# Kernel tuning notes

Measured on AMD Instinct MI355X. Metric: run time of the kernel, lower is better.

Reference implementation:

```python
import jax, jax.numpy as jnp
import numpy as np

SEQ_LEN = 8192
HEAD_DIM = 128


def setup_inputs() -> dict:
    key = jax.random.key(0)
    kq, kk, kv = jax.random.split(key, 3)
    q = jax.random.normal(kq, (SEQ_LEN, HEAD_DIM), dtype=jnp.float32)
    k = jax.random.normal(kk, (SEQ_LEN, HEAD_DIM), dtype=jnp.float32)
    v = jax.random.normal(kv, (SEQ_LEN, HEAD_DIM), dtype=jnp.float32)
    return {"q": q, "k": k, "v": v}


def reference(q, k, v):
    # FlashAttention computes exact softmax attention; the blocked loops with
    # online max/sum rescaling in the source are an exact reformulation of:
    #   O = softmax(Q K^T) V
    # NOTE: the original module applies no 1/sqrt(d) scaling, so neither do we.
    s = jnp.einsum('nd,md->nm', q, k)          # [N, N] scores
    p = jax.nn.softmax(s, axis=-1)             # stable softmax (online in src)
    return jnp.einsum('nm,md->nd', p, v)       # [N, d]
```

## Files before the change

kernel.cpp:

```cpp
#include <hip/hip_runtime.h>

#define N_SEQ 8192
#define HDIM  128

typedef _Float16 half8v  __attribute__((ext_vector_type(8)));
typedef float    floatx16 __attribute__((ext_vector_type(16)));
typedef unsigned int uint32;

__global__ void prep_kv(const float* __restrict__ K, const float* __restrict__ V,
                        _Float16* __restrict__ K16s, _Float16* __restrict__ Vs) {
    __shared__ float Kl[32 * 132];
    __shared__ float Vl[32 * 132];
    const int t  = threadIdx.x;
    const int nt = blockIdx.x;
    const int n0 = nt * 32;
    #pragma unroll
    for (int kk = 0; kk < 4; kk++) {
        int idx = t + 256 * kk;
        int nl = idx >> 5, c4 = idx & 31;
        float4 f = *(((const float4*)(K + (size_t)(n0 + nl) * HDIM)) + c4);
        float* dk = &Kl[nl * 132 + c4 * 4];
        dk[0] = f.x; dk[1] = f.y; dk[2] = f.z; dk[3] = f.w;
        float4 g = *(((const float4*)(V + (size_t)(n0 + nl) * HDIM)) + c4);
        float* dv = &Vl[nl * 132 + c4 * 4];
        dv[0] = g.x; dv[1] = g.y; dv[2] = g.z; dv[3] = g.w;
    }
    __syncthreads();
    #pragma unroll
    for (int rep = 0; rep < 2; rep++) {
        int ch = t + rep * 256;
        int kc = ch >> 6, lane = ch & 63, l31 = lane & 31, q5 = (lane >> 5) & 1;
        half8v h;
        #pragma unroll
        for (int j = 0; j < 8; j++) h[j] = (_Float16)Kl[l31 * 132 + kc * 16 + q5 * 8 + j];
        *(half8v*)(K16s + (((size_t)nt * 8 + kc) * 64 + lane) * 8) = h;
    }
    #pragma unroll
    for (int rep = 0; rep < 2; rep++) {
        int ch = t + rep * 256;
        int dt = ch >> 7, kc2 = (ch >> 6) & 1, lane = ch & 63, l31 = lane & 31, q5 = (lane >> 5) & 1;
        half8v h;
        #pragma unroll
        for (int j = 0; j < 8; j++) h[j] = (_Float16)Vl[(kc2 * 16 + q5 * 8 + j) * 132 + dt * 32 + l31];
        *(half8v*)(Vs + ((((size_t)nt * 4 + dt) * 2 + kc2) * 64 + lane) * 8) = h;
    }
}

static __device__ __forceinline__ void stage_tile(
        const _Float16* __restrict__ K16s, const _Float16* __restrict__ Vs,
        _Float16* lds, size_t nt, int wv, int lane) {
    #pragma unroll
    for (int i = 0; i < 4; i++) {
        const int c = wv * 4 + i;
        const _Float16* base = (c < 8) ? (K16s + (nt * 8 + c) * 512)
                                       : (Vs + (nt * 8 + (size_t)(c - 8)) * 512);
        __builtin_amdgcn_global_load_lds(
            (const __attribute__((address_space(1))) void*)(base + lane * 8),
            (__attribute__((address_space(3))) void*)(lds + c * 512),
            16, 0, 0);
    }
}

static __device__ __forceinline__ void do_pv(const half8v (&vsrc)[8], const uint32 (&hpk)[8],
                                             floatx16 (&oacc)[4], int q5) {
    #pragma unroll
    for (int kc2 = 0; kc2 < 2; kc2++) {
        uint32 pass0 = q5 ? hpk[4 * kc2 + 0] : hpk[4 * kc2 + 2];
        uint32 pass1 = q5 ? hpk[4 * kc2 + 1] : hpk[4 * kc2 + 3];
        uint32 r0 = (uint32)__shfl_xor((int)pass0, 32, 64);
        uint32 r1 = (uint32)__shfl_xor((int)pass1, 32, 64);
        uint32 b0 = q5 ? r0 : hpk[4 * kc2 + 0];
        uint32 b1 = q5 ? r1 : hpk[4 * kc2 + 1];
        uint32 b2 = q5 ? hpk[4 * kc2 + 2] : r0;
        uint32 b3 = q5 ? hpk[4 * kc2 + 3] : r1;
        uint4 bu = make_uint4(b0, b1, b2, b3);
        half8v bfrag = __builtin_bit_cast(half8v, bu);
        #pragma unroll
        for (int dt = 0; dt < 4; dt++)
            oacc[dt] = __builtin_amdgcn_mfma_f32_32x32x16_f16(vsrc[dt * 2 + kc2], bfrag, oacc[dt], 0, 0, 0);
    }
}

template <bool DO_PV>
static __device__ __forceinline__ void pipe_step(
        const half8v (&qf)[8], half8v (&vin)[8], const half8v (&vprev)[8],
        floatx16 (&oacc)[4], uint32 (&hpk)[8],
        float& runm, float& lsum, float& palpha, bool& pflag,
        const _Float16* lds, int lane, int q5) {
    half8v kf[8];
    #pragma unroll
    for (int kc = 0; kc < 8; kc++)
        kf[kc] = *(const half8v*)(lds + kc * 512 + lane * 8);
    #pragma unroll
    for (int j = 0; j < 8; j++)
        vin[j] = *(const half8v*)(lds + (8 + j) * 512 + lane * 8);
    if (pflag) {
        #pragma unroll
        for (int dt = 0; dt < 4; dt++)
            #pragma unroll
            for (int r = 0; r < 16; r++) oacc[dt][r] *= palpha;
        pflag = false;
    }
    if (DO_PV) do_pv(vprev, hpk, oacc, q5);
    floatx16 s0, s1;
    #pragma unroll
    for (int r = 0; r < 16; r++) { s0[r] = 0.0f; s1[r] = 0.0f; }
    #pragma unroll
    for (int kc = 0; kc < 4; kc++)
        s0 = __builtin_amdgcn_mfma_f32_32x32x16_f16(kf[kc], qf[kc], s0, 0, 0, 0);
    #pragma unroll
    for (int kc = 4; kc < 8; kc++)
        s1 = __builtin_amdgcn_mfma_f32_32x32x16_f16(kf[kc], qf[kc], s1, 0, 0, 0);
    float sc[16];
    #pragma unroll
    for (int r = 0; r < 16; r++) sc[r] = s0[r] + s1[r];
    float tm[8];
    #pragma unroll
    for (int r = 0; r < 8; r++) tm[r] = fmaxf(sc[r], sc[r + 8]);
    #pragma unroll
    for (int w = 4; w; w >>= 1)
        #pragma unroll
        for (int r = 0; r < w; r++) tm[r] = fmaxf(tm[r], tm[r + w]);
    float cmax = fmaxf(tm[0], __shfl_xor(tm[0], 32, 64));
    if (__any(cmax > runm + 12.0f)) {
        const float mnew = fmaxf(runm, cmax);
        palpha = __builtin_amdgcn_exp2f(runm - mnew);
        runm = mnew;
        lsum *= palpha;
        pflag = true;
    }
    float p[16];
    #pragma unroll
    for (int r = 0; r < 16; r++) p[r] = __builtin_amdgcn_exp2f(sc[r] - runm);
    float ts[8];
    #pragma unroll
    for (int r = 0; r < 8; r++) ts[r] = p[r] + p[r + 8];
    #pragma unroll
    for (int w = 4; w; w >>= 1)
        #pragma unroll
        for (int r = 0; r < w; r++) ts[r] += ts[r + w];
    lsum += ts[0];
    #pragma unroll
    for (int t2 = 0; t2 < 8; t2++) {
        auto pk = __builtin_amdgcn_cvt_pkrtz(p[2 * t2], p[2 * t2 + 1]);
        hpk[t2] = __builtin_bit_cast(uint32, pk);
    }
}

__launch_bounds__(256, 2)
__global__ void fa_main(const float* __restrict__ Qp, const _Float16* __restrict__ K16s,
                        const _Float16* __restrict__ Vs, float* __restrict__ Opart,
                        float* __restrict__ lpart, float* __restrict__ mpart, int tiles) {
    __shared__ _Float16 ldsbuf[2][8192];
    const int tid  = threadIdx.x;
    const int lane = tid & 63;
    const int wv   = tid >> 6;
    const int l31  = lane & 31;
    const int q5   = lane >> 5;
    const int sp   = blockIdx.x;
    const int m0   = blockIdx.y * 128 + wv * 32;
    const float LOG2E = 1.44269504088896f;

    half8v qf[8];
    {
        const float* qrow = Qp + (size_t)(m0 + l31) * HDIM;
        #pragma unroll
        for (int kc = 0; kc < 8; kc++) {
            const float4 a = *(const float4*)(qrow + kc * 16 + q5 * 8);
            const float4 b = *(const float4*)(qrow + kc * 16 + q5 * 8 + 4);
            half8v h;
            h[0] = (_Float16)(a.x * LOG2E); h[1] = (_Float16)(a.y * LOG2E);
            h[2] = (_Float16)(a.z * LOG2E); h[3] = (_Float16)(a.w * LOG2E);
            h[4] = (_Float16)(b.x * LOG2E); h[5] = (_Float16)(b.y * LOG2E);
            h[6] = (_Float16)(b.z * LOG2E); h[7] = (_Float16)(b.w * LOG2E);
            qf[kc] = h;
        }
    }

    floatx16 oacc[4];
    #pragma unroll
    for (int dt = 0; dt < 4; dt++)
        #pragma unroll
        for (int r = 0; r < 16; r++) oacc[dt][r] = 0.0f;

    float runm = -3.0e38f;
    float lsum = 0.0f;
    float palpha = 0.0f;
    bool  pflag = false;
    uint32 hpk[8];
    half8v va[8], vb[8];

    const size_t nt0 = (size_t)sp * tiles;

    stage_tile(K16s, Vs, ldsbuf[0], nt0, wv, lane);
    __syncthreads();
    stage_tile(K16s, Vs, ldsbuf[1], nt0 + 1, wv, lane);
    pipe_step<false>(qf, va, va, oacc, hpk, runm, lsum, palpha, pflag, ldsbuf[0], lane, q5);
    __syncthreads();
    for (int p = 0; p < (tiles - 2) / 2; p++) {
        stage_tile(K16s, Vs, ldsbuf[0], nt0 + 2 + 2 * p, wv, lane);
        pipe_step<true>(qf, vb, va, oacc, hpk, runm, lsum, palpha, pflag, ldsbuf[1], lane, q5);
        __syncthreads();
        stage_tile(K16s, Vs, ldsbuf[1], nt0 + 3 + 2 * p, wv, lane);
        pipe_step<true>(qf, va, vb, oacc, hpk, runm, lsum, palpha, pflag, ldsbuf[0], lane, q5);
        __syncthreads();
    }
    pipe_step<true>(qf, vb, va, oacc, hpk, runm, lsum, palpha, pflag, ldsbuf[1], lane, q5);
    if (pflag) {
        #pragma unroll
        for (int dt = 0; dt < 4; dt++)
            #pragma unroll
            for (int r = 0; r < 16; r++) oacc[dt][r] *= palpha;
    }
    do_pv(vb, hpk, oacc, q5);

    float ltot = lsum + __shfl_xor(lsum, 32, 64);
    if (lane < 32) {
        lpart[(size_t)sp * N_SEQ + m0 + l31] = ltot;
        mpart[(size_t)sp * N_SEQ + m0 + l31] = runm;
    }

    float* ldsf = (float*)ldsbuf;
    const size_t obase = ((size_t)sp * N_SEQ + blockIdx.y * 128) * HDIM;
    #pragma unroll
    for (int qtr = 0; qtr < 4; qtr++) {
        __syncthreads();
        if (wv == qtr) {
            #pragma unroll
            for (int dt = 0; dt < 4; dt++)
                #pragma unroll
                for (int g = 0; g < 4; g++) {
                    float4 v = make_float4(oacc[dt][4 * g + 0], oacc[dt][4 * g + 1],
                                           oacc[dt][4 * g + 2], oacc[dt][4 * g + 3]);
                    *(float4*)&ldsf[l31 * 132 + dt * 32 + g * 8 + q5 * 4] = v;
                }
        }
        __syncthreads();
        const int lrow = wv * 8 + (lane >> 3);
        const int c    = lane & 7;
        #pragma unroll
        for (int j = 0; j < 4; j++) {
            float4 v = *(const float4*)&ldsf[lrow * 132 + (j * 8 + c) * 4];
            *(float4*)&Opart[obase + (size_t)(qtr * 32 + lrow) * HDIM + (j * 8 + c) * 4] = v;
        }
    }
}

template <int S>
__global__ __launch_bounds__(256) void fa_merge(const float* __restrict__ Opart,
                                                const float* __restrict__ lpart,
                                                const float* __restrict__ mpart,
                                                float* __restrict__ Out) {
    const int t = threadIdx.x;
    const int m = blockIdx.x * 32 + (t >> 3);
    const int c = t & 7;

    float mv[S], lv[S];
    #pragma unroll
    for (int s = 0; s < S; s++) {
        mv[s] = mpart[(size_t)s * N_SEQ + m];
        lv[s] = lpart[(size_t)s * N_SEQ + m];
    }
    float M = -3.0e38f;
    #pragma unroll
    for (int s = 0; s < S; s++) M = fmaxf(M, mv[s]);
    float wsc[S];
    float L = 0.0f;
    #pragma unroll
    for (int s = 0; s < S; s++) {
        wsc[s] = __builtin_amdgcn_exp2f(mv[s] - M);
        L += lv[s] * wsc[s];
    }
    const float inv = 1.0f / L;

    float4 acc[4];
    #pragma unroll
    for (int j = 0; j < 4; j++) acc[j] = make_float4(0.f, 0.f, 0.f, 0.f);
    #pragma unroll
    for (int s = 0; s < S; s++) {
        const float ww = wsc[s] * inv;
        const float* src = Opart + ((size_t)s * N_SEQ + m) * HDIM;
        #pragma unroll
        for (int j = 0; j < 4; j++) {
            float4 v = *(const float4*)&src[(j * 8 + c) * 4];
            acc[j].x += v.x * ww; acc[j].y += v.y * ww;
            acc[j].z += v.z * ww; acc[j].w += v.w * ww;
        }
    }
    float* dst = Out + (size_t)m * HDIM;
    #pragma unroll
    for (int j = 0; j < 4; j++)
        *(float4*)&dst[(j * 8 + c) * 4] = acc[j];
}

__global__ void fa_naive(const float* __restrict__ Q, const float* __restrict__ K,
                         const float* __restrict__ V, float* __restrict__ O) {
    const int m = blockIdx.x;
    const int t = threadIdx.x;
    __shared__ float qs[HDIM];
    __shared__ float ps[256];
    __shared__ float red[256];
    if (t < HDIM) qs[t] = Q[(size_t)m * HDIM + t] * 1.44269504f;
    __syncthreads();
    float om = -3.0e38f, ls = 0.0f, oa = 0.0f;
    for (int nb = 0; nb < N_SEQ; nb += 256) {
        const float* kr = K + (size_t)(nb + t) * HDIM;
        float s = 0.0f;
        #pragma unroll 8
        for (int d = 0; d < HDIM; d++) s += qs[d] * kr[d];
        red[t] = s; __syncthreads();
        for (int st = 128; st > 0; st >>= 1) { if (t < st) red[t] = fmaxf(red[t], red[t + st]); __syncthreads(); }
        float cm = red[0];
        __syncthreads();
        float mn = fmaxf(om, cm);
        float al = __builtin_amdgcn_exp2f(om - mn);
        om = mn;
        float pp = __builtin_amdgcn_exp2f(s - mn);
        ps[t] = pp; red[t] = pp; __syncthreads();
        for (int st = 128; st > 0; st >>= 1) { if (t < st) red[t] += red[t + st]; __syncthreads(); }
        float csum = red[0];
        ls = ls * al + csum;
        if (t < HDIM) {
            float acc = 0.0f;
            for (int j = 0; j < 256; j++) acc += ps[j] * V[(size_t)(nb + j) * HDIM + t];
            oa = oa * al + acc;
        }
        __syncthreads();
    }
    if (t < HDIM) O[(size_t)m * HDIM + t] = oa / ls;
}

extern "C" void kernel_launch(void* const* d_in, const int* in_sizes, int n_in,
                              void* d_out, int out_size, void* d_ws, size_t ws_size,
                              hipStream_t stream) {
    const float* q = (const float*)d_in[0];
    const float* k = (const float*)d_in[1];
    const float* v = (const float*)d_in[2];
    float* out = (float*)d_out;

    const size_t MB = 1024ull * 1024ull;
    int S = 0;
    for (int s = 8; s >= 1; s >>= 1) {
        size_t need = 4 * MB + (size_t)s * (4 * MB + 64 * 1024);
        if (ws_size >= need) { S = s; break; }
    }
    if (S == 0) {
        fa_naive<<<N_SEQ, 256, 0, stream>>>(q, k, v, out);
        return;
    }
    char* ws = (char*)d_ws;
    _Float16* K16s = (_Float16*)ws;
    _Float16* Vs   = (_Float16*)(ws + 2 * MB);
    float* Opart   = (float*)(ws + 4 * MB);
    float* lpart   = (float*)(ws + 4 * MB + (size_t)S * 4 * MB);
    float* mpart   = lpart + (size_t)S * N_SEQ;

    prep_kv<<<dim3(N_SEQ / 32), dim3(256), 0, stream>>>(k, v, K16s, Vs);
    fa_main<<<dim3(S, N_SEQ / 128), dim3(256), 0, stream>>>(q, K16s, Vs, Opart, lpart, mpart, (N_SEQ / 32) / S);
    dim3 mg(N_SEQ / 32);
    switch (S) {
        case 8:  fa_merge<8> <<<mg, dim3(256), 0, stream>>>(Opart, lpart, mpart, out); break;
        case 4:  fa_merge<4> <<<mg, dim3(256), 0, stream>>>(Opart, lpart, mpart, out); break;
        case 2:  fa_merge<2> <<<mg, dim3(256), 0, stream>>>(Opart, lpart, mpart, out); break;
        default: fa_merge<1> <<<mg, dim3(256), 0, stream>>>(Opart, lpart, mpart, out); break;
    }
}
```

Baseline: 120.8 us.

## Triple-buffer K/V LDS staging with partial waitcnt barriers and widen merge grid

```diff
diff --git a/kernel.cpp b/kernel.cpp
--- a/kernel.cpp
+++ b/kernel.cpp
@@ -147,11 +147,16 @@
     }
 }
 
+static __device__ __forceinline__ void phase_sync() {
+    asm volatile("s_waitcnt vmcnt(4) lgkmcnt(0)" ::: "memory");
+    __builtin_amdgcn_s_barrier();
+}
+
 __launch_bounds__(256, 2)
 __global__ void fa_main(const float* __restrict__ Qp, const _Float16* __restrict__ K16s,
                         const _Float16* __restrict__ Vs, float* __restrict__ Opart,
                         float* __restrict__ lpart, float* __restrict__ mpart, int tiles) {
-    __shared__ _Float16 ldsbuf[2][8192];
+    __shared__ _Float16 ldsbuf[3][8192];
     const int tid  = threadIdx.x;
     const int lane = tid & 63;
     const int wv   = tid >> 6;
@@ -191,21 +196,37 @@
     half8v va[8], vb[8];
 
     const size_t nt0 = (size_t)sp * tiles;
-
-    stage_tile(K16s, Vs, ldsbuf[0], nt0, wv, lane);
-    __syncthreads();
-    stage_tile(K16s, Vs, ldsbuf[1], nt0 + 1, wv, lane);
-    pipe_step<false>(qf, va, va, oacc, hpk, runm, lsum, palpha, pflag, ldsbuf[0], lane, q5);
-    __syncthreads();
+    _Float16* lb = &ldsbuf[0][0];
+    const int last = tiles - 1;
+
+    stage_tile(K16s, Vs, lb + 0 * 8192, nt0 + 0, wv, lane);
+    stage_tile(K16s, Vs, lb + 1 * 8192, nt0 + 1, wv, lane);
+
+    phase_sync();
+    stage_tile(K16s, Vs, lb + 2 * 8192, nt0 + 2, wv, lane);
+    pipe_step<false>(qf, va, va, oacc, hpk, runm, lsum, palpha, pflag, lb, lane, q5);
+
+    int cs = 1;
+    int ps = 0;
     for (int p = 0; p < (tiles - 2) / 2; p++) {
-        stage_tile(K16s, Vs, ldsbuf[0], nt0 + 2 + 2 * p, wv, lane);
-        pipe_step<true>(qf, vb, va, oacc, hpk, runm, lsum, palpha, pflag, ldsbuf[1], lane, q5);
-        __syncthreads();
-        stage_tile(K16s, Vs, ldsbuf[1], nt0 + 3 + 2 * p, wv, lane);
-        pipe_step<true>(qf, va, vb, oacc, hpk, runm, lsum, palpha, pflag, ldsbuf[0], lane, q5);
-        __syncthreads();
-    }
-    pipe_step<true>(qf, vb, va, oacc, hpk, runm, lsum, palpha, pflag, ldsbuf[1], lane, q5);
+        const int t1 = 1 + 2 * p;
+        phase_sync();
+        {
+            int st = t1 + 2; if (st > last) st = last;
+            stage_tile(K16s, Vs, lb + ps * 8192, nt0 + st, wv, lane);
+        }
+        pipe_step<true>(qf, vb, va, oacc, hpk, runm, lsum, palpha, pflag, lb + cs * 8192, lane, q5);
+        ps = cs; cs = (cs + 1 == 3) ? 0 : cs + 1;
+        phase_sync();
+        {
+            int st = t1 + 3; if (st > last) st = last;
+            stage_tile(K16s, Vs, lb + ps * 8192, nt0 + st, wv, lane);
+        }
+        pipe_step<true>(qf, va, vb, oacc, hpk, runm, lsum, palpha, pflag, lb + cs * 8192, lane, q5);
+        ps = cs; cs = (cs + 1 == 3) ? 0 : cs + 1;
+    }
+    phase_sync();
+    pipe_step<true>(qf, vb, va, oacc, hpk, runm, lsum, palpha, pflag, lb + cs * 8192, lane, q5);
     if (pflag) {
         #pragma unroll
         for (int dt = 0; dt < 4; dt++)
@@ -219,6 +240,8 @@
         lpart[(size_t)sp * N_SEQ + m0 + l31] = ltot;
         mpart[(size_t)sp * N_SEQ + m0 + l31] = runm;
     }
+
+    asm volatile("s_waitcnt vmcnt(0)" ::: "memory");
 
     float* ldsf = (float*)ldsbuf;
     const size_t obase = ((size_t)sp * N_SEQ + blockIdx.y * 128) * HDIM;
@@ -252,8 +275,8 @@
                                                 const float* __restrict__ mpart,
                                                 float* __restrict__ Out) {
     const int t = threadIdx.x;
-    const int m = blockIdx.x * 32 + (t >> 3);
-    const int c = t & 7;
+    const int m = blockIdx.x * 16 + (t >> 4);
+    const int c = t & 15;
 
     float mv[S], lv[S];
     #pragma unroll
@@ -273,24 +296,24 @@
     }
     const float inv = 1.0f / L;
 
-    float4 acc[4];
-    #pragma unroll
-    for (int j = 0; j < 4; j++) acc[j] = make_float4(0.f, 0.f, 0.f, 0.f);
+    float4 acc[2];
+    #pragma unroll
+    for (int j = 0; j < 2; j++) acc[j] = make_float4(0.f, 0.f, 0.f, 0.f);
     #pragma unroll
     for (int s = 0; s < S; s++) {
         const float ww = wsc[s] * inv;
         const float* src = Opart + ((size_t)s * N_SEQ + m) * HDIM;
         #pragma unroll
-        for (int j = 0; j < 4; j++) {
-            float4 v = *(const float4*)&src[(j * 8 + c) * 4];
+        for (int j = 0; j < 2; j++) {
+            float4 v = *(const float4*)&src[(j * 16 + c) * 4];
             acc[j].x += v.x * ww; acc[j].y += v.y * ww;
             acc[j].z += v.z * ww; acc[j].w += v.w * ww;
         }
     }
     float* dst = Out + (size_t)m * HDIM;
     #pragma unroll
-    for (int j = 0; j < 4; j++)
-        *(float4*)&dst[(j * 8 + c) * 4] = acc[j];
+    for (int j = 0; j < 2; j++)
+        *(float4*)&dst[(j * 16 + c) * 4] = acc[j];
 }
 
 __global__ void fa_naive(const float* __restrict__ Q, const float* __restrict__ K,
@@ -357,7 +380,7 @@
 
     prep_kv<<<dim3(N_SEQ / 32), dim3(256), 0, stream>>>(k, v, K16s, Vs);
     fa_main<<<dim3(S, N_SEQ / 128), dim3(256), 0, stream>>>(q, K16s, Vs, Opart, lpart, mpart, (N_SEQ / 32) / S);
-    dim3 mg(N_SEQ / 32);
+    dim3 mg(N_SEQ / 16);
     switch (S) {
         case 8:  fa_merge<8> <<<mg, dim3(256), 0, stream>>>(Opart, lpart, mpart, out); break;
         case 4:  fa_merge<4> <<<mg, dim3(256), 0, stream>>>(Opart, lpart, mpart, out); break;
```

New measurement: 122.0 us. About the same (+1.0%).

## Fuse K/V prep, attention and split merge into one persistent kernel

Applied to the files above, without the earlier changes.

```diff
diff --git a/kernel.cpp b/kernel.cpp
--- a/kernel.cpp
+++ b/kernel.cpp
@@ -6,45 +6,6 @@
 typedef _Float16 half8v  __attribute__((ext_vector_type(8)));
 typedef float    floatx16 __attribute__((ext_vector_type(16)));
 typedef unsigned int uint32;
-
-__global__ void prep_kv(const float* __restrict__ K, const float* __restrict__ V,
-                        _Float16* __restrict__ K16s, _Float16* __restrict__ Vs) {
-    __shared__ float Kl[32 * 132];
-    __shared__ float Vl[32 * 132];
-    const int t  = threadIdx.x;
-    const int nt = blockIdx.x;
-    const int n0 = nt * 32;
-    #pragma unroll
-    for (int kk = 0; kk < 4; kk++) {
-        int idx = t + 256 * kk;
-        int nl = idx >> 5, c4 = idx & 31;
-        float4 f = *(((const float4*)(K + (size_t)(n0 + nl) * HDIM)) + c4);
-        float* dk = &Kl[nl * 132 + c4 * 4];
-        dk[0] = f.x; dk[1] = f.y; dk[2] = f.z; dk[3] = f.w;
-        float4 g = *(((const float4*)(V + (size_t)(n0 + nl) * HDIM)) + c4);
-        float* dv = &Vl[nl * 132 + c4 * 4];
-        dv[0] = g.x; dv[1] = g.y; dv[2] = g.z; dv[3] = g.w;
-    }
-    __syncthreads();
-    #pragma unroll
-    for (int rep = 0; rep < 2; rep++) {
-        int ch = t + rep * 256;
-        int kc = ch >> 6, lane = ch & 63, l31 = lane & 31, q5 = (lane >> 5) & 1;
-        half8v h;
-        #pragma unroll
-        for (int j = 0; j < 8; j++) h[j] = (_Float16)Kl[l31 * 132 + kc * 16 + q5 * 8 + j];
-        *(half8v*)(K16s + (((size_t)nt * 8 + kc) * 64 + lane) * 8) = h;
-    }
-    #pragma unroll
-    for (int rep = 0; rep < 2; rep++) {
-        int ch = t + rep * 256;
-        int dt = ch >> 7, kc2 = (ch >> 6) & 1, lane = ch & 63, l31 = lane & 31, q5 = (lane >> 5) & 1;
-        half8v h;
-        #pragma unroll
-        for (int j = 0; j < 8; j++) h[j] = (_Float16)Vl[(kc2 * 16 + q5 * 8 + j) * 132 + dt * 32 + l31];
-        *(half8v*)(Vs + ((((size_t)nt * 4 + dt) * 2 + kc2) * 64 + lane) * 8) = h;
-    }
-}
 
 static __device__ __forceinline__ void stage_tile(
         const _Float16* __restrict__ K16s, const _Float16* __restrict__ Vs,
@@ -148,10 +109,14 @@
 }
 
 __launch_bounds__(256, 2)
-__global__ void fa_main(const float* __restrict__ Qp, const _Float16* __restrict__ K16s,
-                        const _Float16* __restrict__ Vs, float* __restrict__ Opart,
-                        float* __restrict__ lpart, float* __restrict__ mpart, int tiles) {
-    __shared__ _Float16 ldsbuf[2][8192];
+__global__ void fa_all(const float* __restrict__ Qp, const float* __restrict__ K,
+                       const float* __restrict__ V,
+                       _Float16* __restrict__ K16s, _Float16* __restrict__ Vs,
+                       float* __restrict__ Opart,
+                       float* __restrict__ lpart, float* __restrict__ mpart,
+                       int* __restrict__ counters, float* __restrict__ Out, int tiles) {
+    __shared__ float smem_f[8448];
+    __shared__ int flag_s;
     const int tid  = threadIdx.x;
     const int lane = tid & 63;
     const int wv   = tid >> 6;
@@ -159,7 +124,49 @@
     const int q5   = lane >> 5;
     const int sp   = blockIdx.x;
     const int m0   = blockIdx.y * 128 + wv * 32;
+    const int nb   = gridDim.x * gridDim.y;
+    const int lid  = blockIdx.y * gridDim.x + blockIdx.x;
     const float LOG2E = 1.44269504088896f;
+    int* prep_ctr = counters + 64;
+
+    {
+        float* Kl = smem_f;
+        float* Vl = smem_f + 4224;
+        for (int tl = lid; tl < N_SEQ / 32; tl += nb) {
+            const int n0 = tl * 32;
+            #pragma unroll
+            for (int kk = 0; kk < 4; kk++) {
+                int idx = tid + 256 * kk;
+                int nl = idx >> 5, c4 = idx & 31;
+                float4 f = *(((const float4*)(K + (size_t)(n0 + nl) * HDIM)) + c4);
+                float* dk = &Kl[nl * 132 + c4 * 4];
+                dk[0] = f.x; dk[1] = f.y; dk[2] = f.z; dk[3] = f.w;
+                float4 g = *(((const float4*)(V + (size_t)(n0 + nl) * HDIM)) + c4);
+                float* dv = &Vl[nl * 132 + c4 * 4];
+                dv[0] = g.x; dv[1] = g.y; dv[2] = g.z; dv[3] = g.w;
+            }
+            __syncthreads();
+            #pragma unroll
+            for (int rep = 0; rep < 2; rep++) {
+                int ch = tid + rep * 256;
+                int kc = ch >> 6, ln = ch & 63, r31 = ln & 31, rq5 = (ln >> 5) & 1;
+                half8v h;
+                #pragma unroll
+                for (int j = 0; j < 8; j++) h[j] = (_Float16)Kl[r31 * 132 + kc * 16 + rq5 * 8 + j];
+                *(half8v*)(K16s + (((size_t)tl * 8 + kc) * 64 + ln) * 8) = h;
+            }
+            #pragma unroll
+            for (int rep = 0; rep < 2; rep++) {
+                int ch = tid + rep * 256;
+                int dt = ch >> 7, kc2 = (ch >> 6) & 1, ln = ch & 63, r31 = ln & 31, rq5 = (ln >> 5) & 1;
+                half8v h;
+                #pragma unroll
+                for (int j = 0; j < 8; j++) h[j] = (_Float16)Vl[(kc2 * 16 + rq5 * 8 + j) * 132 + dt * 32 + r31];
+                *(half8v*)(Vs + ((((size_t)tl * 4 + dt) * 2 + kc2) * 64 + ln) * 8) = h;
+            }
+            __syncthreads();
+        }
+    }
 
     half8v qf[8];
     {
@@ -177,6 +184,17 @@
         }
     }
 
+    if (tid == 0) {
+        __threadfence();
+        atomicAdd(prep_ctr, 1);
+        while (atomicAdd(prep_ctr, 0) < nb) __builtin_amdgcn_s_sleep(8);
+    }
+    __syncthreads();
+    __threadfence();
+
+    _Float16* ldsbuf0 = (_Float16*)smem_f;
+    _Float16* ldsbuf1 = ldsbuf0 + 8192;
+
     floatx16 oacc[4];
     #pragma unroll
     for (int dt = 0; dt < 4; dt++)
@@ -192,20 +210,20 @@
 
     const size_t nt0 = (size_t)sp * tiles;
 
-    stage_tile(K16s, Vs, ldsbuf[0], nt0, wv, lane);
-    __syncthreads();
-    stage_tile(K16s, Vs, ldsbuf[1], nt0 + 1, wv, lane);
-    pipe_step<false>(qf, va, va, oacc, hpk, runm, lsum, palpha, pflag, ldsbuf[0], lane, q5);
+    stage_tile(K16s, Vs, ldsbuf0, nt0, wv, lane);
+    __syncthreads();
+    stage_tile(K16s, Vs, ldsbuf1, nt0 + 1, wv, lane);
+    pipe_step<false>(qf, va, va, oacc, hpk, runm, lsum, palpha, pflag, ldsbuf0, lane, q5);
     __syncthreads();
     for (int p = 0; p < (tiles - 2) / 2; p++) {
-        stage_tile(K16s, Vs, ldsbuf[0], nt0 + 2 + 2 * p, wv, lane);
-        pipe_step<true>(qf, vb, va, oacc, hpk, runm, lsum, palpha, pflag, ldsbuf[1], lane, q5);
-        __syncthreads();
-        stage_tile(K16s, Vs, ldsbuf[1], nt0 + 3 + 2 * p, wv, lane);
-        pipe_step<true>(qf, va, vb, oacc, hpk, runm, lsum, palpha, pflag, ldsbuf[0], lane, q5);
-        __syncthreads();
-    }
-    pipe_step<true>(qf, vb, va, oacc, hpk, runm, lsum, palpha, pflag, ldsbuf[1], lane, q5);
+        stage_tile(K16s, Vs, ldsbuf0, nt0 + 2 + 2 * p, wv, lane);
+        pipe_step<true>(qf, vb, va, oacc, hpk, runm, lsum, palpha, pflag, ldsbuf1, lane, q5);
+        __syncthreads();
+        stage_tile(K16s, Vs, ldsbuf1, nt0 + 3 + 2 * p, wv, lane);
+        pipe_step<true>(qf, va, vb, oacc, hpk, runm, lsum, palpha, pflag, ldsbuf0, lane, q5);
+        __syncthreads();
+    }
+    pipe_step<true>(qf, vb, va, oacc, hpk, runm, lsum, palpha, pflag, ldsbuf1, lane, q5);
     if (pflag) {
         #pragma unroll
         for (int dt = 0; dt < 4; dt++)
@@ -220,7 +238,7 @@
         mpart[(size_t)sp * N_SEQ + m0 + l31] = runm;
     }
 
-    float* ldsf = (float*)ldsbuf;
+    float* ldsf = smem_f;
     const size_t obase = ((size_t)sp * N_SEQ + blockIdx.y * 128) * HDIM;
     #pragma unroll
     for (int qtr = 0; qtr < 4; qtr++) {
@@ -244,53 +262,52 @@
             *(float4*)&Opart[obase + (size_t)(qtr * 32 + lrow) * HDIM + (j * 8 + c) * 4] = v;
         }
     }
-}
-
-template <int S>
-__global__ __launch_bounds__(256) void fa_merge(const float* __restrict__ Opart,
-                                                const float* __restrict__ lpart,
-                                                const float* __restrict__ mpart,
-                                                float* __restrict__ Out) {
-    const int t = threadIdx.x;
-    const int m = blockIdx.x * 32 + (t >> 3);
-    const int c = t & 7;
-
-    float mv[S], lv[S];
-    #pragma unroll
-    for (int s = 0; s < S; s++) {
-        mv[s] = mpart[(size_t)s * N_SEQ + m];
-        lv[s] = lpart[(size_t)s * N_SEQ + m];
-    }
-    float M = -3.0e38f;
-    #pragma unroll
-    for (int s = 0; s < S; s++) M = fmaxf(M, mv[s]);
-    float wsc[S];
-    float L = 0.0f;
-    #pragma unroll
-    for (int s = 0; s < S; s++) {
-        wsc[s] = __builtin_amdgcn_exp2f(mv[s] - M);
-        L += lv[s] * wsc[s];
-    }
-    const float inv = 1.0f / L;
-
-    float4 acc[4];
-    #pragma unroll
-    for (int j = 0; j < 4; j++) acc[j] = make_float4(0.f, 0.f, 0.f, 0.f);
-    #pragma unroll
-    for (int s = 0; s < S; s++) {
-        const float ww = wsc[s] * inv;
-        const float* src = Opart + ((size_t)s * N_SEQ + m) * HDIM;
-        #pragma unroll
-        for (int j = 0; j < 4; j++) {
-            float4 v = *(const float4*)&src[(j * 8 + c) * 4];
-            acc[j].x += v.x * ww; acc[j].y += v.y * ww;
-            acc[j].z += v.z * ww; acc[j].w += v.w * ww;
-        }
-    }
-    float* dst = Out + (size_t)m * HDIM;
-    #pragma unroll
-    for (int j = 0; j < 4; j++)
-        *(float4*)&dst[(j * 8 + c) * 4] = acc[j];
+
+    __syncthreads();
+    if (tid == 0) {
+        __threadfence();
+        int old = atomicAdd(&counters[blockIdx.y], 1);
+        flag_s = (old == (int)gridDim.x - 1);
+    }
+    __syncthreads();
+    if (!flag_s) return;
+    __threadfence();
+
+    const int S   = gridDim.x;
+    const int ym0 = blockIdx.y * 128;
+    const int rg  = tid >> 4;
+    const int c   = tid & 15;
+    for (int rr = 0; rr < 8; rr++) {
+        const int m = ym0 + rr * 16 + rg;
+        float mv[8], lv[8];
+        #pragma unroll
+        for (int s = 0; s < 8; s++)
+            if (s < S) { mv[s] = mpart[(size_t)s * N_SEQ + m]; lv[s] = lpart[(size_t)s * N_SEQ + m]; }
+        float M = -3.0e38f;
+        #pragma unroll
+        for (int s = 0; s < 8; s++) if (s < S) M = fmaxf(M, mv[s]);
+        float wsc[8];
+        float L = 0.0f;
+        #pragma unroll
+        for (int s = 0; s < 8; s++)
+            if (s < S) { wsc[s] = __builtin_amdgcn_exp2f(mv[s] - M); L += lv[s] * wsc[s]; }
+        const float inv = 1.0f / L;
+        float4 a0 = make_float4(0.f, 0.f, 0.f, 0.f);
+        float4 a1 = make_float4(0.f, 0.f, 0.f, 0.f);
+        #pragma unroll
+        for (int s = 0; s < 8; s++)
+            if (s < S) {
+                const float ww = wsc[s] * inv;
+                const float* src = Opart + ((size_t)s * N_SEQ + m) * HDIM;
+                float4 v = *(const float4*)&src[c * 4];
+                a0.x += v.x * ww; a0.y += v.y * ww; a0.z += v.z * ww; a0.w += v.w * ww;
+                v = *(const float4*)&src[(16 + c) * 4];
+                a1.x += v.x * ww; a1.y += v.y * ww; a1.z += v.z * ww; a1.w += v.w * ww;
+            }
+        float* dst = Out + (size_t)m * HDIM;
+        *(float4*)&dst[c * 4]        = a0;
+        *(float4*)&dst[(16 + c) * 4] = a1;
+    }
 }
 
 __global__ void fa_naive(const float* __restrict__ Q, const float* __restrict__ K,
@@ -341,7 +358,7 @@
     const size_t MB = 1024ull * 1024ull;
     int S = 0;
     for (int s = 8; s >= 1; s >>= 1) {
-        size_t need = 4 * MB + (size_t)s * (4 * MB + 64 * 1024);
+        size_t need = 4 * MB + (size_t)s * (4 * MB + 64 * 1024) + 4096;
         if (ws_size >= need) { S = s; break; }
     }
     if (S == 0) {
@@ -354,14 +371,9 @@
     float* Opart   = (float*)(ws + 4 * MB);
     float* lpart   = (float*)(ws + 4 * MB + (size_t)S * 4 * MB);
     float* mpart   = lpart + (size_t)S * N_SEQ;
-
-    prep_kv<<<dim3(N_SEQ / 32), dim3(256), 0, stream>>>(k, v, K16s, Vs);
-    fa_main<<<dim3(S, N_SEQ / 128), dim3(256), 0, stream>>>(q, K16s, Vs, Opart, lpart, mpart, (N_SEQ / 32) / S);
-    dim3 mg(N_SEQ / 32);
-    switch (S) {
-        case 8:  fa_merge<8> <<<mg, dim3(256), 0, stream>>>(Opart, lpart, mpart, out); break;
-        case 4:  fa_merge<4> <<<mg, dim3(256), 0, stream>>>(Opart, lpart, mpart, out); break;
-        case 2:  fa_merge<2> <<<mg, dim3(256), 0, stream>>>(Opart, lpart, mpart, out); break;
-        default: fa_merge<1> <<<mg, dim3(256), 0, stream>>>(Opart, lpart, mpart, out); break;
-    }
-}
+    int*   counters = (int*)(mpart + (size_t)S * N_SEQ);
+
+    hipMemsetAsync(counters, 0, 65 * sizeof(int), stream);
+    fa_all<<<dim3(S, N_SEQ / 128), dim3(256), 0, stream>>>(
+        q, k, v, K16s, Vs, Opart, lpart, mpart, counters, out, (N_SEQ / 32) / S);
+}
```

Result: slower. 228.4 us (+89.0%).

## Process two KV tiles per phase and drop the software-pipelined PV stage

Applied to the files above, without the earlier changes.

```diff
diff --git a/kernel.cpp b/kernel.cpp
--- a/kernel.cpp
+++ b/kernel.cpp
@@ -81,27 +81,14 @@
     }
 }
 
-template <bool DO_PV>
-static __device__ __forceinline__ void pipe_step(
-        const half8v (&qf)[8], half8v (&vin)[8], const half8v (&vprev)[8],
-        floatx16 (&oacc)[4], uint32 (&hpk)[8],
-        float& runm, float& lsum, float& palpha, bool& pflag,
+static __device__ __forceinline__ void step64(
+        const half8v (&qf)[8], floatx16 (&oacc)[4],
+        float& runm, float& lsum,
         const _Float16* lds, int lane, int q5) {
     half8v kf[8];
     #pragma unroll
     for (int kc = 0; kc < 8; kc++)
         kf[kc] = *(const half8v*)(lds + kc * 512 + lane * 8);
-    #pragma unroll
-    for (int j = 0; j < 8; j++)
-        vin[j] = *(const half8v*)(lds + (8 + j) * 512 + lane * 8);
-    if (pflag) {
-        #pragma unroll
-        for (int dt = 0; dt < 4; dt++)
-            #pragma unroll
-            for (int r = 0; r < 16; r++) oacc[dt][r] *= palpha;
-        pflag = false;
-    }
-    if (DO_PV) do_pv(vprev, hpk, oacc, q5);
     floatx16 s0, s1;
     #pragma unroll
     for (int r = 0; r < 16; r++) { s0[r] = 0.0f; s1[r] = 0.0f; }
@@ -111,12 +98,27 @@
     #pragma unroll
     for (int kc = 4; kc < 8; kc++)
         s1 = __builtin_amdgcn_mfma_f32_32x32x16_f16(kf[kc], qf[kc], s1, 0, 0, 0);
-    float sc[16];
-    #pragma unroll
-    for (int r = 0; r < 16; r++) sc[r] = s0[r] + s1[r];
+    float sA[16];
+    #pragma unroll
+    for (int r = 0; r < 16; r++) sA[r] = s0[r] + s1[r];
+    #pragma unroll
+    for (int kc = 0; kc < 8; kc++)
+        kf[kc] = *(const half8v*)(lds + 8192 + kc * 512 + lane * 8);
+    #pragma unroll
+    for (int r = 0; r < 16; r++) { s0[r] = 0.0f; s1[r] = 0.0f; }
+    #pragma unroll
+    for (int kc = 0; kc < 4; kc++)
+        s0 = __builtin_amdgcn_mfma_f32_32x32x16_f16(kf[kc], qf[kc], s0, 0, 0, 0);
+    #pragma unroll
+    for (int kc = 4; kc < 8; kc++)
+        s1 = __builtin_amdgcn_mfma_f32_32x32x16_f16(kf[kc], qf[kc], s1, 0, 0, 0);
+    float sB[16];
+    #pragma unroll
+    for (int r = 0; r < 16; r++) sB[r] = s0[r] + s1[r];
     float tm[8];
     #pragma unroll
-    for (int r = 0; r < 8; r++) tm[r] = fmaxf(sc[r], sc[r + 8]);
+    for (int r = 0; r < 8; r++)
+        tm[r] = fmaxf(fmaxf(sA[r], sA[r + 8]), fmaxf(sB[r], sB[r + 8]));
     #pragma unroll
     for (int w = 4; w; w >>= 1)
         #pragma unroll
@@ -124,34 +126,50 @@
     float cmax = fmaxf(tm[0], __shfl_xor(tm[0], 32, 64));
     if (__any(cmax > runm + 12.0f)) {
         const float mnew = fmaxf(runm, cmax);
-        palpha = __builtin_amdgcn_exp2f(runm - mnew);
+        const float alpha = __builtin_amdgcn_exp2f(runm - mnew);
+        #pragma unroll
+        for (int dt = 0; dt < 4; dt++)
+            #pragma unroll
+            for (int r = 0; r < 16; r++) oacc[dt][r] *= alpha;
+        lsum *= alpha;
         runm = mnew;
-        lsum *= palpha;
-        pflag = true;
-    }
-    float p[16];
-    #pragma unroll
-    for (int r = 0; r < 16; r++) p[r] = __builtin_amdgcn_exp2f(sc[r] - runm);
+    }
+    float pA[16], pB[16];
+    #pragma unroll
+    for (int r = 0; r < 16; r++) pA[r] = __builtin_amdgcn_exp2f(sA[r] - runm);
+    #pragma unroll
+    for (int r = 0; r < 16; r++) pB[r] = __builtin_amdgcn_exp2f(sB[r] - runm);
     float ts[8];
     #pragma unroll
-    for (int r = 0; r < 8; r++) ts[r] = p[r] + p[r + 8];
+    for (int r = 0; r < 8; r++) ts[r] = (pA[r] + pA[r + 8]) + (pB[r] + pB[r + 8]);
     #pragma unroll
     for (int w = 4; w; w >>= 1)
         #pragma unroll
         for (int r = 0; r < w; r++) ts[r] += ts[r + w];
     lsum += ts[0];
+    uint32 hA[8], hB[8];
     #pragma unroll
     for (int t2 = 0; t2 < 8; t2++) {
-        auto pk = __builtin_amdgcn_cvt_pkrtz(p[2 * t2], p[2 * t2 + 1]);
-        hpk[t2] = __builtin_bit_cast(uint32, pk);
-    }
+        auto ka = __builtin_amdgcn_cvt_pkrtz(pA[2 * t2], pA[2 * t2 + 1]);
+        hA[t2] = __builtin_bit_cast(uint32, ka);
+        auto kb = __builtin_amdgcn_cvt_pkrtz(pB[2 * t2], pB[2 * t2 + 1]);
+        hB[t2] = __builtin_bit_cast(uint32, kb);
+    }
+    #pragma unroll
+    for (int j = 0; j < 8; j++)
+        kf[j] = *(const half8v*)(lds + (8 + j) * 512 + lane * 8);
+    do_pv(kf, hA, oacc, q5);
+    #pragma unroll
+    for (int j = 0; j < 8; j++)
+        kf[j] = *(const half8v*)(lds + 8192 + (8 + j) * 512 + lane * 8);
+    do_pv(kf, hB, oacc, q5);
 }
 
 __launch_bounds__(256, 2)
 __global__ void fa_main(const float* __restrict__ Qp, const _Float16* __restrict__ K16s,
                         const _Float16* __restrict__ Vs, float* __restrict__ Opart,
                         float* __restrict__ lpart, float* __restrict__ mpart, int tiles) {
-    __shared__ _Float16 ldsbuf[2][8192];
+    __shared__ _Float16 ldsbuf[2][16384];
     const int tid  = threadIdx.x;
     const int lane = tid & 63;
     const int wv   = tid >> 6;
@@ -185,34 +203,23 @@
 
     float runm = -3.0e38f;
     float lsum = 0.0f;
-    float palpha = 0.0f;
-    bool  pflag = false;
-    uint32 hpk[8];
-    half8v va[8], vb[8];
 
     const size_t nt0 = (size_t)sp * tiles;
-
-    stage_tile(K16s, Vs, ldsbuf[0], nt0, wv, lane);
+    const int phases = tiles >> 1;
+
+    stage_tile(K16s, Vs, ldsbuf[0], nt0 + 0, wv, lane);
+    stage_tile(K16s, Vs, ldsbuf[0] + 8192, nt0 + 1, wv, lane);
     __syncthreads();
-    stage_tile(K16s, Vs, ldsbuf[1], nt0 + 1, wv, lane);
-    pipe_step<false>(qf, va, va, oacc, hpk, runm, lsum, palpha, pflag, ldsbuf[0], lane, q5);
-    __syncthreads();
-    for (int p = 0; p < (tiles - 2) / 2; p++) {
-        stage_tile(K16s, Vs, ldsbuf[0], nt0 + 2 + 2 * p, wv, lane);
-        pipe_step<true>(qf, vb, va, oacc, hpk, runm, lsum, palpha, pflag, ldsbuf[1], lane, q5);
-        __syncthreads();
-        stage_tile(K16s, Vs, ldsbuf[1], nt0 + 3 + 2 * p, wv, lane);
-        pipe_step<true>(qf, va, vb, oacc, hpk, runm, lsum, palpha, pflag, ldsbuf[0], lane, q5);
-        __syncthreads();
-    }
-    pipe_step<true>(qf, vb, va, oacc, hpk, runm, lsum, palpha, pflag, ldsbuf[1], lane, q5);
-    if (pflag) {
-        #pragma unroll
-        for (int dt = 0; dt < 4; dt++)
-            #pragma unroll
-            for (int r = 0; r < 16; r++) oacc[dt][r] *= palpha;
-    }
-    do_pv(vb, hpk, oacc, q5);
+    for (int ph = 0; ph < phases; ph++) {
+        _Float16* cur = ldsbuf[ph & 1];
+        _Float16* nxt = ldsbuf[(ph & 1) ^ 1];
+        if (ph + 1 < phases) {
+            stage_tile(K16s, Vs, nxt, nt0 + 2 * ph + 2, wv, lane);
+            stage_tile(K16s, Vs, nxt + 8192, nt0 + 2 * ph + 3, wv, lane);
+        }
+        step64(qf, oacc, runm, lsum, cur, lane, q5);
+        __syncthreads();
+    }
 
     float ltot = lsum + __shfl_xor(lsum, 32, 64);
     if (lane < 32) {
@@ -252,8 +259,8 @@
                                                 const float* __restrict__ mpart,
                                                 float* __restrict__ Out) {
     const int t = threadIdx.x;
-    const int m = blockIdx.x * 32 + (t >> 3);
-    const int c = t & 7;
+    const int m = blockIdx.x * 16 + (t >> 4);
+    const int c = t & 15;
 
     float mv[S], lv[S];
     #pragma unroll
@@ -273,24 +280,24 @@
     }
     const float inv = 1.0f / L;
 
-    float4 acc[4];
-    #pragma unroll
-    for (int j = 0; j < 4; j++) acc[j] = make_float4(0.f, 0.f, 0.f, 0.f);
+    float4 acc[2];
+    #pragma unroll
+    for (int j = 0; j < 2; j++) acc[j] = make_float4(0.f, 0.f, 0.f, 0.f);
     #pragma unroll
     for (int s = 0; s < S; s++) {
         const float ww = wsc[s] * inv;
         const float* src = Opart + ((size_t)s * N_SEQ + m) * HDIM;
         #pragma unroll
-        for (int j = 0; j < 4; j++) {
-            float4 v = *(const float4*)&src[(j * 8 + c) * 4];
+        for (int j = 0; j < 2; j++) {
+            float4 v = *(const float4*)&src[(j * 16 + c) * 4];
             acc[j].x += v.x * ww; acc[j].y += v.y * ww;
             acc[j].z += v.z * ww; acc[j].w += v.w * ww;
         }
     }
     float* dst = Out + (size_t)m * HDIM;
     #pragma unroll
-    for (int j = 0; j < 4; j++)
-        *(float4*)&dst[(j * 8 + c) * 4] = acc[j];
+    for (int j = 0; j < 2; j++)
+        *(float4*)&dst[(j * 16 + c) * 4] = acc[j];
 }
 
 __global__ void fa_naive(const float* __restrict__ Q, const float* __restrict__ K,
@@ -357,7 +364,7 @@
 
     prep_kv<<<dim3(N_SEQ / 32), dim3(256), 0, stream>>>(k, v, K16s, Vs);
     fa_main<<<dim3(S, N_SEQ / 128), dim3(256), 0, stream>>>(q, K16s, Vs, Opart, lpart, mpart, (N_SEQ / 32) / S);
-    dim3 mg(N_SEQ / 32);
+    dim3 mg(N_SEQ / 16);
     switch (S) {
         case 8:  fa_merge<8> <<<mg, dim3(256), 0, stream>>>(Opart, lpart, mpart, out); break;
         case 4:  fa_merge<4> <<<mg, dim3(256), 0, stream>>>(Opart, lpart, mpart, out); break;
```

Result: no change. 119.5 us (-1.1%).
